# Kernel tuning notes

Hardware: AMD Instinct MI355X
Metric: run time of the kernel (lower is better)

## Reference

```python
import jax, jax.numpy as jnp
import numpy as np

DN = ('NCHW', 'OIHW', 'NCHW')

def conv3x3(x, w):
    return jax.lax.conv_general_dilated(x, w, (1, 1), ((1, 1), (1, 1)), dimension_numbers=DN)

def dsc(x, w1, w2):
    # DynamicSparseConv: per-sample per-channel softmax 3x3 depthwise kernel + residual
    B, C, H, W = x.shape
    pooled = x.mean(axis=(2, 3))                                  # [B, C] (AdaptiveAvgPool2d(1))
    h = jax.nn.gelu(pooled @ w1.T, approximate=False)             # [B, Cr] (1x1 conv == matmul)
    logits = (h @ w2.T).reshape(B, C, 9)                          # [B, C, 9]
    wk = jax.nn.softmax(logits, axis=2)
    # 3x3 patches: [B, C*9, H, W], feature dim ordered (C, kh, kw)
    patches = jax.lax.conv_general_dilated_patches(x, (3, 3), (1, 1), ((1, 1), (1, 1)))
    patches = patches.reshape(B, C, 9, H, W)
    out = jnp.einsum('bckhw,bck->bchw', patches, wk)
    return out + x

def pixel_shuffle(x, r):
    B, C, H, W = x.shape
    c = C // (r * r)
    return x.reshape(B, c, r, r, H, W).transpose(0, 1, 4, 2, 5, 3).reshape(B, c, H * r, W * r)

def setup_inputs() -> dict:
    key = jax.random.key(0)
    ks = jax.random.split(key, 12)
    B, C, H, W, OUT = 16, 128, 64, 64, 64
    CR = max(4, C // 8)            # 16
    RE = max(4, OUT // 8)          # 8
    s = 0.05
    return {
        'x1': jax.random.normal(ks[0], (B, C, H, W), jnp.float32),
        'x2': jax.random.normal(ks[1], (B, C, H, W), jnp.float32),
        'd1_w1': jax.random.normal(ks[2], (CR, C), jnp.float32) * s,
        'd1_w2': jax.random.normal(ks[3], (9 * C, CR), jnp.float32) * s,
        'd2_w1': jax.random.normal(ks[4], (CR, C), jnp.float32) * s,
        'd2_w2': jax.random.normal(ks[5], (9 * C, CR), jnp.float32) * s,
        'align_w': jax.random.normal(ks[6], (C, 2 * C), jnp.float32) * s,
        'up_w1': jax.random.normal(ks[7], (4 * C, C, 3, 3), jnp.float32) * s,
        'up_w2': jax.random.normal(ks[8], (OUT, C), jnp.float32) * s,
        're_w1': jax.random.normal(ks[9], (RE, OUT, 3, 3), jnp.float32) * s,
        're_w2': jax.random.normal(ks[10], (OUT, RE, 3, 3), jnp.float32) * s,
    }

def reference(x1, x2, d1_w1, d1_w2, d2_w1, d2_w2, align_w, up_w1, up_w2, re_w1, re_w2):
    def dynamic_block(x):  # shared weights for both inputs (same nn.Sequential)
        x = dsc(x, d1_w1, d1_w2)
        x = jax.nn.relu(x)
        return dsc(x, d2_w1, d2_w2)
    a = dynamic_block(x1)
    b = dynamic_block(x2)
    fused = jnp.einsum('bchw,oc->bohw', jnp.concatenate([a, b], axis=1), align_w)  # 1x1 conv
    u = conv3x3(fused, up_w1)            # [B, 4C, H, W]
    u = pixel_shuffle(u, 2)              # [B, C, 2H, 2W]
    up = jnp.einsum('bchw,oc->bohw', u, up_w2)  # [B, OUT, 2H, 2W]
    re = conv3x3(jax.nn.relu(conv3x3(up, re_w1)), re_w2)
    return up + re
```

## Files before the change

kernel.cpp:

```cpp
#include <hip/hip_runtime.h>
#include <math.h>

typedef unsigned short ushort;
typedef short bf16x8 __attribute__((ext_vector_type(8)));
typedef ushort us8 __attribute__((ext_vector_type(8)));
typedef float f32x16 __attribute__((ext_vector_type(16)));
typedef float f32x4 __attribute__((ext_vector_type(4)));

static const size_t OFF_POOLED = 0;
static const size_t OFF_WK     = 4096;
static const size_t OFF_WT     = 40960;
static const size_t OFF_WF     = 188416;
static const size_t OFF_AW1    = 204800;
static const size_t OFF_AW2    = 209408;
static const size_t OFF_T      = 262144;
static const size_t OFF_AB     = 8650752;
static const size_t OFF_F      = 17039360;

static __device__ __forceinline__ ushort f2bf(float f) {
    unsigned int u = __builtin_bit_cast(unsigned int, f);
    u += 0x7FFF + ((u >> 16) & 1);
    return (ushort)(u >> 16);
}
static __device__ __forceinline__ float bf2f(ushort u) {
    return __builtin_bit_cast(float, ((unsigned int)u) << 16);
}

__global__ __launch_bounds__(256) void head_kernel(const float* __restrict__ x1,
                                                   const float* __restrict__ x2,
                                                   float* __restrict__ pooled,
                                                   const float* __restrict__ up_w1,
                                                   const float* __restrict__ up_w2,
                                                   ushort* __restrict__ Awt,
                                                   const float* __restrict__ align_w,
                                                   ushort* __restrict__ Wf,
                                                   const float* __restrict__ re_w1,
                                                   ushort* __restrict__ Aw1,
                                                   const float* __restrict__ re_w2,
                                                   ushort* __restrict__ Aw2) {
    const int bid = blockIdx.x;
    const int t = threadIdx.x;
    if (bid < 4096) {
        int bc = bid;
        const float* x = (bc >> 11) ? x2 : x1;
        const float4* p = (const float4*)(x + (size_t)(bc & 2047) * 4096);
        float s = 0.f;
        for (int i = t; i < 1024; i += 256) {
            float4 v = p[i];
            s += v.x + v.y + v.z + v.w;
        }
        #pragma unroll
        for (int off = 32; off; off >>= 1) s += __shfl_down(s, off);
        __shared__ float r4[4];
        if ((t & 63) == 0) r4[t >> 6] = s;
        __syncthreads();
        if (t == 0) pooled[bc] = (r4[0] + r4[1] + r4[2] + r4[3]) * (1.f / 4096.f);
    } else if (bid < 5248) {
        int idx = (bid - 4096) * 256 + t;
        int j = idx & 7;
        int lane = (idx >> 3) & 63;
        int mt = (idx >> 9) & 3;
        int mh = (idx >> 11) & 1;
        int s = idx >> 12;
        int tap = s >> 3, c16 = s & 7;
        int arow = lane & 31;
        int o_sem = (mt & 1) * 32 + (arow & 3) + 4 * ((arow >> 3) & 3) + 16 * ((arow >> 2) & 1);
        int ph = 2 * mh + (mt >> 1);
        int cin = c16 * 16 + (lane >> 5) * 8 + j;
        float acc = 0.f;
        #pragma unroll 4
        for (int c = 0; c < 128; c++)
            acc += up_w2[o_sem * 128 + c] * up_w1[((size_t)(c * 4 + ph) * 128 + cin) * 9 + tap];
        Awt[idx] = f2bf(acc);
    } else if (bid == 5248) {
        #pragma unroll 1
        for (int i = 0; i < 16; i++) {
            int tk = t + (i << 8);
            int step = tk >> 8, mt = (tk >> 6) & 3, lane = tk & 63;
            int o = mt * 32 + (lane & 31);
            int cb = step * 16 + (lane >> 5) * 8;
            #pragma unroll
            for (int j = 0; j < 8; j++) Wf[(size_t)tk * 8 + j] = f2bf(align_w[o * 256 + cb + j]);
        }
    } else if (bid < 5285) {
        int idx = (bid - 5249) * 256 + t;
        if (idx < 9216) {
            int j = idx & 7, lane = (idx >> 3) & 63, s = idx >> 9;
            int m = lane & 15, kq = lane >> 4;
            int tap = s >> 1, ch = s & 1;
            int cin = ch * 32 + kq * 8 + j;
            float v = (m < 8) ? re_w1[((size_t)(m * 64 + cin)) * 9 + tap] : 0.f;
            Aw1[idx] = f2bf(v);
        }
    } else {
        int idx = (bid - 5285) * 256 + t;
        if (idx < 5120) {
            int j = idx & 7, lane = (idx >> 3) & 63, mt = (idx >> 9) & 1, s = idx >> 10;
            int m = mt * 32 + (lane & 31), half = lane >> 5;
            int k = s * 16 + half * 8 + j;
            int tap = k >> 3, c = k & 7;
            float v = (tap < 9) ? re_w2[((size_t)(m * 8 + c)) * 9 + tap] : 0.f;
            Aw2[idx] = f2bf(v);
        }
    }
}

__global__ __launch_bounds__(256) void dsc1_kernel(const float* __restrict__ x1,
                                                   const float* __restrict__ x2,
                                                   const float* __restrict__ pooled,
                                                   const float* __restrict__ w1,
                                                   const float* __restrict__ w2,
                                                   ushort* __restrict__ y,
                                                   float* __restrict__ pooled2) {
    int bc = blockIdx.x;
    const float* xp = ((bc >> 11) ? x2 : x1) + (size_t)(bc & 2047) * 4096;
    ushort* yp = y + (size_t)bc * 4096;
    __shared__ float tile[66 * 66];
    __shared__ float r4[4];
    __shared__ float sp[128];
    __shared__ float sh[16];
    __shared__ float lgs[9];
    int t = threadIdx.x;
    if (t < 128) sp[t] = pooled[(bc >> 7) * 128 + t];
    for (int i = t; i < 66 * 66; i += 256) tile[i] = 0.f;
    __syncthreads();
    if (t < 16) {
        float a = 0.f;
        #pragma unroll 4
        for (int c = 0; c < 128; c++) a += w1[t * 128 + c] * sp[c];
        sh[t] = 0.5f * a * (1.f + erff(a * 0.70710678118654752f));
    }
    const float4* xp4 = (const float4*)xp;
    for (int i = t; i < 1024; i += 256) {
        float4 v = xp4[i];
        int h = i >> 4, w = (i & 15) * 4;
        float* d = &tile[(h + 1) * 66 + w + 1];
        d[0] = v.x; d[1] = v.y; d[2] = v.z; d[3] = v.w;
    }
    __syncthreads();
    if (t < 9) {
        float a = 0.f;
        const float* wr = w2 + (size_t)((bc & 127) * 9 + t) * 16;
        #pragma unroll
        for (int r = 0; r < 16; r++) a += wr[r] * sh[r];
        lgs[t] = a;
    }
    __syncthreads();
    float kk[9];
    {
        float m = -INFINITY;
        #pragma unroll
        for (int k = 0; k < 9; k++) m = fmaxf(m, lgs[k]);
        float se = 0.f;
        #pragma unroll
        for (int k = 0; k < 9; k++) { kk[k] = expf(lgs[k] - m); se += kk[k]; }
        float inv = 1.f / se;
        #pragma unroll
        for (int k = 0; k < 9; k++) kk[k] *= inv;
    }
    float psum = 0.f;
    for (int i = t * 2; i < 4096; i += 512) {
        int h = i >> 6, w = i & 63;
        const float* c = &tile[h * 66 + w];
        float v0 = kk[0]*c[0] + kk[1]*c[1] + kk[2]*c[2]
                 + kk[3]*c[66] + kk[4]*c[67] + kk[5]*c[68]
                 + kk[6]*c[132] + kk[7]*c[133] + kk[8]*c[134] + c[67];
        float v1 = kk[0]*c[1] + kk[1]*c[2] + kk[2]*c[3]
                 + kk[3]*c[67] + kk[4]*c[68] + kk[5]*c[69]
                 + kk[6]*c[133] + kk[7]*c[134] + kk[8]*c[135] + c[68];
        v0 = fmaxf(v0, 0.f); v1 = fmaxf(v1, 0.f);
        psum += v0 + v1;
        ushort2 pk = {f2bf(v0), f2bf(v1)};
        *(ushort2*)&yp[i] = pk;
    }
    #pragma unroll
    for (int off = 32; off; off >>= 1) psum += __shfl_down(psum, off);
    if ((t & 63) == 0) r4[t >> 6] = psum;
    __syncthreads();
    if (t == 0) pooled2[bc] = (r4[0] + r4[1] + r4[2] + r4[3]) * (1.f / 4096.f);
}

__global__ __launch_bounds__(256) void dsc2_kernel(const ushort* __restrict__ x,
                                                   const float* __restrict__ pooled,
                                                   const float* __restrict__ w1,
                                                   const float* __restrict__ w2,
                                                   ushort* __restrict__ y) {
    int bc = blockIdx.x;
    const ushort* xp = x + (size_t)bc * 4096;
    ushort* yp = y + (size_t)bc * 4096;
    __shared__ float tile[66 * 66];
    __shared__ float sp[128];
    __shared__ float sh[16];
    __shared__ float lgs[9];
    int t = threadIdx.x;
    if (t < 128) sp[t] = pooled[(bc >> 7) * 128 + t];
    for (int i = t; i < 66 * 66; i += 256) tile[i] = 0.f;
    __syncthreads();
    if (t < 16) {
        float a = 0.f;
        #pragma unroll 4
        for (int c = 0; c < 128; c++) a += w1[t * 128 + c] * sp[c];
        sh[t] = 0.5f * a * (1.f + erff(a * 0.70710678118654752f));
    }
    for (int i = t; i < 512; i += 256) {
        int4 raw = *(const int4*)&xp[i * 8];
        const ushort* u = (const ushort*)&raw;
        int h = i >> 3, w = (i & 7) * 8;
        float* d = &tile[(h + 1) * 66 + w + 1];
        #pragma unroll
        for (int j = 0; j < 8; j++) d[j] = bf2f(u[j]);
    }
    __syncthreads();
    if (t < 9) {
        float a = 0.f;
        const float* wr = w2 + (size_t)((bc & 127) * 9 + t) * 16;
        #pragma unroll
        for (int r = 0; r < 16; r++) a += wr[r] * sh[r];
        lgs[t] = a;
    }
    __syncthreads();
    float kk[9];
    {
        float m = -INFINITY;
        #pragma unroll
        for (int k = 0; k < 9; k++) m = fmaxf(m, lgs[k]);
        float se = 0.f;
        #pragma unroll
        for (int k = 0; k < 9; k++) { kk[k] = expf(lgs[k] - m); se += kk[k]; }
        float inv = 1.f / se;
        #pragma unroll
        for (int k = 0; k < 9; k++) kk[k] *= inv;
    }
    for (int i = t * 2; i < 4096; i += 512) {
        int h = i >> 6, w = i & 63;
        const float* c = &tile[h * 66 + w];
        float v0 = kk[0]*c[0] + kk[1]*c[1] + kk[2]*c[2]
                 + kk[3]*c[66] + kk[4]*c[67] + kk[5]*c[68]
                 + kk[6]*c[132] + kk[7]*c[133] + kk[8]*c[134] + c[67];
        float v1 = kk[0]*c[1] + kk[1]*c[2] + kk[2]*c[3]
                 + kk[3]*c[67] + kk[4]*c[68] + kk[5]*c[69]
                 + kk[6]*c[133] + kk[7]*c[134] + kk[8]*c[135] + c[68];
        ushort2 pk = {f2bf(v0), f2bf(v1)};
        *(ushort2*)&yp[i] = pk;
    }
}

__global__ __launch_bounds__(256, 2) void align_mfma_kernel(const ushort* __restrict__ A,
                                                            const ushort* __restrict__ Bv,
                                                            const ushort* __restrict__ Wf,
                                                            ushort* __restrict__ F) {
    __shared__ ushort Xs[2 * 128 * 8];
    const int b = blockIdx.y;
    const int px0 = blockIdx.x << 7;
    const int tid = threadIdx.x;
    const int wave = tid >> 6, lane = tid & 63;
    const int l31 = lane & 31, half = lane >> 5;

    f32x16 acc[4];
    #pragma unroll
    for (int mt = 0; mt < 4; mt++)
        #pragma unroll
        for (int r = 0; r < 16; r++) acc[mt][r] = 0.f;

    const int cg0 = tid >> 7, pxs0 = tid & 127;
    const int bfofs = (wave * 32 + l31) * 8 + half * 1024;

    for (int step = 0; step < 16; step++) {
        const ushort* src =
            (step < 8 ? A : Bv) + (((size_t)(b * 128 + (step & 7) * 16)) << 12) + px0;
        if (step) __syncthreads();
        #pragma unroll
        for (int q = 0; q < 2; q++) {
            int cg = cg0 + q * 2, px = pxs0;
            ushort v0 = src[((size_t)(cg * 4 + 0) << 12) + px];
            ushort v1 = src[((size_t)(cg * 4 + 1) << 12) + px];
            ushort v2 = src[((size_t)(cg * 4 + 2) << 12) + px];
            ushort v3 = src[((size_t)(cg * 4 + 3) << 12) + px];
            ushort4 pk = {v0, v1, v2, v3};
            *(ushort4*)&Xs[(cg >> 1) * 1024 + px * 8 + (cg & 1) * 4] = pk;
        }
        __syncthreads();
        bf16x8 bfrag = *(const bf16x8*)&Xs[bfofs];
        const bf16x8* wf = (const bf16x8*)(Wf + ((size_t)step * 4 * 64 + lane) * 8);
        #pragma unroll
        for (int mt = 0; mt < 4; mt++)
            acc[mt] = __builtin_amdgcn_mfma_f32_32x32x16_bf16(wf[mt * 64], bfrag, acc[mt], 0, 0, 0);
    }
    ushort* fp = F + ((size_t)(b * 4096 + px0 + wave * 32 + l31)) * 128;
    #pragma unroll
    for (int mt = 0; mt < 4; mt++) {
        #pragma unroll
        for (int g = 0; g < 4; g++) {
            ushort4 pk = {f2bf(acc[mt][g * 4 + 0]), f2bf(acc[mt][g * 4 + 1]),
                          f2bf(acc[mt][g * 4 + 2]), f2bf(acc[mt][g * 4 + 3])};
            *(ushort4*)(fp + mt * 32 + half * 4 + 8 * g) = pk;
        }
    }
}

__global__ __launch_bounds__(512, 4) void up_mfma_kernel(const ushort* __restrict__ F,
                                                         const ushort* __restrict__ Awt,
                                                         ushort* __restrict__ U) {
    __shared__ ushort Xs[180 * 128];
    const int b = blockIdx.y;
    const int tr = blockIdx.x >> 3, tc = blockIdx.x & 7;
    const int tid = threadIdx.x;
    const int wave = tid >> 6, lane = tid & 63;
    const int l31 = lane & 31, half = lane >> 5;
    const int mh = wave >> 2, bmt = (wave >> 1) & 1, nh = wave & 1;

    for (int idx = tid; idx < 2880; idx += 512) {
        int px = idx >> 4, q = idx & 15;
        int r = px / 10, c = px - r * 10;
        int gh = tr * 16 - 1 + r, gw = tc * 8 - 1 + c;
        int4 v = {0, 0, 0, 0};
        if ((unsigned)gh < 64u && (unsigned)gw < 64u)
            v = *(const int4*)(F + ((size_t)(b * 4096 + gh * 64 + gw)) * 128 + q * 8);
        *(int4*)&Xs[px * 128 + ((q ^ (px & 7)) << 3)] = v;
    }
    __syncthreads();

    f32x16 acc[2][2];
    #pragma unroll
    for (int mt = 0; mt < 2; mt++)
        #pragma unroll
        for (int nt = 0; nt < 2; nt++)
            #pragma unroll
            for (int r = 0; r < 16; r++) acc[mt][nt][r] = 0.f;

    int xpos[2];
    #pragma unroll
    for (int nt = 0; nt < 2; nt++) {
        int pxl = nh * 64 + nt * 32 + l31;
        xpos[nt] = (pxl >> 3) * 10 + (pxl & 7);
    }

    const ushort* abase = Awt + (size_t)(mh * 4 + bmt * 2) * 512 + lane * 8;

    #define LDA(ss, mtl) (*(const bf16x8*)(abase + (size_t)(ss) * 4096 + (mtl) * 512))
    #define LDB(ss, nt) ({                                                   \
        int tap_ = (ss) >> 3, c16_ = (ss) & 7;                               \
        int ky_ = (tap_ * 11) >> 5;                      \
        int kx_ = tap_ - ky_ * 3;                                            \
        int p_ = xpos[nt] + ky_ * 10 + kx_;                                  \
        int qq_ = c16_ * 2 + half;                                           \
        *(const bf16x8*)&Xs[p_ * 128 + ((qq_ ^ (p_ & 7)) << 3)];             \
    })

    bf16x8 A0[2], A1[2], B0[2], B1[2];
    A0[0] = LDA(0, 0); A0[1] = LDA(0, 1);
    A1[0] = LDA(1, 0); A1[1] = LDA(1, 1);
    B0[0] = LDB(0, 0); B0[1] = LDB(0, 1);
    B1[0] = LDB(1, 0); B1[1] = LDB(1, 1);

    #define SUBSTEP(ASET, BSET, sn)                                                  \
    {                                                                                \
        _Pragma("unroll")                                                            \
        for (int mt = 0; mt < 2; mt++) {                                             \
            acc[mt][0] = __builtin_amdgcn_mfma_f32_32x32x16_bf16(ASET[mt], BSET[0], acc[mt][0], 0, 0, 0); \
            acc[mt][1] = __builtin_amdgcn_mfma_f32_32x32x16_bf16(ASET[mt], BSET[1], acc[mt][1], 0, 0, 0); \
        }                                                                            \
        ASET[0] = LDA(sn, 0); ASET[1] = LDA(sn, 1);                                  \
        BSET[0] = LDB(sn, 0); BSET[1] = LDB(sn, 1);                                  \
    }

    #pragma unroll 2
    for (int s = 0; s < 70; s += 2) {
        SUBSTEP(A0, B0, s + 2)
        int s3 = (s + 3 < 72) ? s + 3 : 0;
        SUBSTEP(A1, B1, s3)
    }
    #pragma unroll
    for (int mt = 0; mt < 2; mt++) {
        acc[mt][0] = __builtin_amdgcn_mfma_f32_32x32x16_bf16(A0[mt], B0[0], acc[mt][0], 0, 0, 0);
        acc[mt][1] = __builtin_amdgcn_mfma_f32_32x32x16_bf16(A0[mt], B0[1], acc[mt][1], 0, 0, 0);
    }
    #pragma unroll
    for (int mt = 0; mt < 2; mt++) {
        acc[mt][0] = __builtin_amdgcn_mfma_f32_32x32x16_bf16(A1[mt], B1[0], acc[mt][0], 0, 0, 0);
        acc[mt][1] = __builtin_amdgcn_mfma_f32_32x32x16_bf16(A1[mt], B1[1], acc[mt][1], 0, 0, 0);
    }
    #undef SUBSTEP
    #undef LDA
    #undef LDB

    #pragma unroll
    for (int nt = 0; nt < 2; nt++) {
        int pxl = nh * 64 + nt * 32 + l31;
        int Y = 2 * (tr * 16 + (pxl >> 3)) + mh;
        int X = 2 * (tc * 8 + (pxl & 7)) + bmt;
        #pragma unroll
        for (int mt = 0; mt < 2; mt++) {
            ushort* up = U + ((size_t)((b * 128 + Y) * 128 + X)) * 64
                       + mt * 32 + half * 16;
            us8 p0, p1;
            #pragma unroll
            for (int i = 0; i < 8; i++) {
                p0[i] = f2bf(acc[mt][nt][i]);
                p1[i] = f2bf(acc[mt][nt][8 + i]);
            }
            *(us8*)up = p0;
            *(us8*)(up + 8) = p1;
        }
    }
}

__global__ __launch_bounds__(256, 2) void re1_kernel(const ushort* __restrict__ U,
                                                     const ushort* __restrict__ Aw1,
                                                     ushort* __restrict__ R1) {
    __shared__ ushort Xs[324 * 72];
    __shared__ ushort As[18 * 64 * 8];
    const int b = blockIdx.y;
    const int ty = blockIdx.x >> 3, tx = blockIdx.x & 7;
    const int tid = threadIdx.x;
    const int wave = tid >> 6, lane = tid & 63;
    const int m16 = lane & 15, kq = lane >> 4;

    for (int idx = tid; idx < 1152; idx += 256)
        *(int4*)&As[idx * 8] = *(const int4*)(Aw1 + (size_t)idx * 8);
    for (int idx = tid; idx < 2592; idx += 256) {
        int px = idx >> 3, q = idx & 7;
        int r = px / 18, c = px - r * 18;
        int gY = ty * 16 - 1 + r, gX = tx * 16 - 1 + c;
        int4 v = {0, 0, 0, 0};
        if ((unsigned)gY < 128u && (unsigned)gX < 128u)
            v = *(const int4*)(U + ((size_t)((b * 128 + gY) * 128 + gX)) * 64 + q * 8);
        *(int4*)&Xs[px * 72 + q * 8] = v;
    }
    __syncthreads();

    f32x4 acc[4];
    #pragma unroll
    for (int nt = 0; nt < 4; nt++)
        #pragma unroll
        for (int r = 0; r < 4; r++) acc[nt][r] = 0.f;

    #pragma unroll 1
    for (int s = 0; s < 18; s++) {
        bf16x8 a = *(const bf16x8*)&As[(s * 64 + lane) * 8];
        int tap = s >> 1, ch = s & 1;
        int ky = tap / 3, kx = tap - ky * 3;
        int xo = (ky * 18 + kx) * 72 + ch * 32 + kq * 8;
        #pragma unroll
        for (int nt = 0; nt < 4; nt++) {
            int row = wave * 4 + nt;
            bf16x8 bv = *(const bf16x8*)&Xs[(row * 18 + m16) * 72 + xo];
            acc[nt] = __builtin_amdgcn_mfma_f32_16x16x32_bf16(a, bv, acc[nt], 0, 0, 0);
        }
    }
    if (kq < 2) {
        #pragma unroll
        for (int nt = 0; nt < 4; nt++) {
            int gY = ty * 16 + wave * 4 + nt, gX = tx * 16 + m16;
            ushort4 pk = {f2bf(fmaxf(acc[nt][0], 0.f)), f2bf(fmaxf(acc[nt][1], 0.f)),
                          f2bf(fmaxf(acc[nt][2], 0.f)), f2bf(fmaxf(acc[nt][3], 0.f))};
            *(ushort4*)(R1 + ((size_t)((b * 128 + gY) * 128 + gX)) * 8 + kq * 4) = pk;
        }
    }
}

__global__ __launch_bounds__(256, 2) void re2_kernel(const ushort* __restrict__ R1,
                                                     const ushort* __restrict__ U,
                                                     const ushort* __restrict__ Aw2,
                                                     float* __restrict__ out) {
    __shared__ ushort Xs[324 * 8];
    __shared__ ushort As[5 * 2 * 64 * 8];
    __shared__ ushort Us[256 * 68];
    const int b = blockIdx.y;
    const int ty = blockIdx.x >> 3, tx = blockIdx.x & 7;
    const int tid = threadIdx.x;
    const int wave = tid >> 6, lane = tid & 63;
    const int l31 = lane & 31, half = lane >> 5;

    for (int idx = tid; idx < 640; idx += 256)
        *(int4*)&As[idx * 8] = *(const int4*)(Aw2 + (size_t)idx * 8);
    for (int idx = tid; idx < 324; idx += 256) {
        int r = idx / 18, c = idx - r * 18;
        int gY = ty * 16 - 1 + r, gX = tx * 16 - 1 + c;
        int4 v = {0, 0, 0, 0};
        if ((unsigned)gY < 128u && (unsigned)gX < 128u)
            v = *(const int4*)(R1 + ((size_t)((b * 128 + gY) * 128 + gX)) * 8);
        *(int4*)&Xs[idx * 8] = v;
    }
    for (int idx = tid; idx < 2048; idx += 256) {
        int px = idx >> 3, q = idx & 7;
        int gY = ty * 16 + (px >> 4), gX = tx * 16 + (px & 15);
        const ushort* s = U + ((size_t)((b * 128 + gY) * 128 + gX)) * 64 + q * 8;
        ushort4 v0 = *(const ushort4*)s;
        ushort4 v1 = *(const ushort4*)(s + 4);
        *(ushort4*)&Us[px * 68 + q * 8] = v0;
        *(ushort4*)&Us[px * 68 + q * 8 + 4] = v1;
    }
    __syncthreads();

    f32x16 acc[2][2];
    #pragma unroll
    for (int mt = 0; mt < 2; mt++)
        #pragma unroll
        for (int nt = 0; nt < 2; nt++)
            #pragma unroll
            for (int r = 0; r < 16; r++) acc[mt][nt][r] = 0.f;

    #pragma unroll
    for (int s = 0; s < 5; s++) {
        bf16x8 a0 = *(const bf16x8*)&As[((s * 2 + 0) * 64 + lane) * 8];
        bf16x8 a1 = *(const bf16x8*)&As[((s * 2 + 1) * 64 + lane) * 8];
        int t = 2 * s + half;
        if (t > 8) t = 8;
        int ky = t / 3, kx = t - ky * 3;
        #pragma unroll
        for (int nt = 0; nt < 2; nt++) {
            int pxl = wave * 64 + nt * 32 + l31;
            int row = pxl >> 4, col = pxl & 15;
            bf16x8 bv = *(const bf16x8*)&Xs[((row + ky) * 18 + col + kx) * 8];
            acc[0][nt] = __builtin_amdgcn_mfma_f32_32x32x16_bf16(a0, bv, acc[0][nt], 0, 0, 0);
            acc[1][nt] = __builtin_amdgcn_mfma_f32_32x32x16_bf16(a1, bv, acc[1][nt], 0, 0, 0);
        }
    }
    #pragma unroll
    for (int mt = 0; mt < 2; mt++) {
        #pragma unroll
        for (int nt = 0; nt < 2; nt++) {
            int pxl = wave * 64 + nt * 32 + l31;
            int gY = ty * 16 + (pxl >> 4), gX = tx * 16 + (pxl & 15);
            #pragma unroll
            for (int r = 0; r < 16; r++) {
                int o = mt * 32 + (r & 3) + 8 * (r >> 2) + 4 * half;
                float v = acc[mt][nt][r] + bf2f(Us[pxl * 68 + o]);
                out[((size_t)(b * 64 + o) * 128 + gY) * 128 + gX] = v;
            }
        }
    }
}

extern "C" void kernel_launch(void* const* d_in, const int* in_sizes, int n_in,
                              void* d_out, int out_size, void* d_ws, size_t ws_size,
                              hipStream_t stream) {
    const float* x1      = (const float*)d_in[0];
    const float* x2      = (const float*)d_in[1];
    const float* d1_w1   = (const float*)d_in[2];
    const float* d1_w2   = (const float*)d_in[3];
    const float* d2_w1   = (const float*)d_in[4];
    const float* d2_w2   = (const float*)d_in[5];
    const float* align_w = (const float*)d_in[6];
    const float* up_w1   = (const float*)d_in[7];
    const float* up_w2   = (const float*)d_in[8];
    const float* re_w1   = (const float*)d_in[9];
    const float* re_w2   = (const float*)d_in[10];
    float* out = (float*)d_out;
    float* ws  = (float*)d_ws;

    float*  pooled  = ws + OFF_POOLED;
    float*  pooled2 = ws + OFF_WK;
    ushort* Awt    = (ushort*)(ws + OFF_WT);
    ushort* Wf     = (ushort*)(ws + OFF_WF);
    ushort* Aw1    = (ushort*)(ws + OFF_AW1);
    ushort* Aw2    = (ushort*)(ws + OFF_AW2);
    ushort* bufT   = (ushort*)(ws + OFF_T);
    ushort* R1     = (ushort*)(ws + OFF_T);
    ushort* bufAB  = (ushort*)(ws + OFF_AB);
    ushort* bufU   = (ushort*)(ws + OFF_AB);
    ushort* F      = (ushort*)(ws + OFF_F);

    head_kernel<<<5305, 256, 0, stream>>>(x1, x2, pooled, up_w1, up_w2, Awt,
                                          align_w, Wf, re_w1, Aw1, re_w2, Aw2);
    dsc1_kernel<<<4096, 256, 0, stream>>>(x1, x2, pooled, d1_w1, d1_w2, bufT, pooled2);
    dsc2_kernel<<<4096, 256, 0, stream>>>(bufT, pooled2, d2_w1, d2_w2, bufAB);

    align_mfma_kernel<<<dim3(32, 16), 256, 0, stream>>>(bufAB, bufAB + 8388608, Wf, F);
    up_mfma_kernel<<<dim3(32, 16), 512, 0, stream>>>(F, Awt, bufU);
    re1_kernel<<<dim3(64, 16), 256, 0, stream>>>(bufU, Aw1, R1);
    re2_kernel<<<dim3(64, 16), 256, 0, stream>>>(R1, bufU, Aw2, out);
}
```

Baseline: 328.3 us.

## Stage weight-fold operands in LDS and compute eight outputs per thread

The head kernel's up_w2×up_w1 weight-folding section is rewritten so each block stages the relevant up_w2 rows and a tap-specific slice of up_w1 into shared memory, then each thread accumulates eight outputs from LDS instead of doing strided global loads per output. This cuts the block count for that section from 1152 to 144 and removes the redundant, uncoalesced global reads. In exchange every head block now declares about 48KB of shared memory, which may reduce occupancy for the pooling blocks that share the kernel. Each block also reads up_w1 with a filter that discards most loaded values.

```diff
diff --git a/kernel.cpp b/kernel.cpp
--- a/kernel.cpp
+++ b/kernel.cpp
@@ -38,6 +38,7 @@
                                                    ushort* __restrict__ Aw1,
                                                    const float* __restrict__ re_w2,
                                                    ushort* __restrict__ Aw2) {
+    __shared__ float sm[12352];
     const int bid = blockIdx.x;
     const int t = threadIdx.x;
     if (bid < 4096) {
@@ -51,28 +52,52 @@
         }
         #pragma unroll
         for (int off = 32; off; off >>= 1) s += __shfl_down(s, off);
-        __shared__ float r4[4];
-        if ((t & 63) == 0) r4[t >> 6] = s;
+        if ((t & 63) == 0) sm[t >> 6] = s;
         __syncthreads();
-        if (t == 0) pooled[bc] = (r4[0] + r4[1] + r4[2] + r4[3]) * (1.f / 4096.f);
-    } else if (bid < 5248) {
-        int idx = (bid - 4096) * 256 + t;
-        int j = idx & 7;
-        int lane = (idx >> 3) & 63;
-        int mt = (idx >> 9) & 3;
-        int mh = (idx >> 11) & 1;
-        int s = idx >> 12;
+        if (t == 0) pooled[bc] = (sm[0] + sm[1] + sm[2] + sm[3]) * (1.f / 4096.f);
+    } else if (bid < 4240) {
+        int w = bid - 4096;
+        int mh = (w >= 72) ? 1 : 0;
+        int s = w - mh * 72;
         int tap = s >> 3, c16 = s & 7;
-        int arow = lane & 31;
-        int o_sem = (mt & 1) * 32 + (arow & 3) + 4 * ((arow >> 3) & 3) + 16 * ((arow >> 2) & 1);
-        int ph = 2 * mh + (mt >> 1);
-        int cin = c16 * 16 + (lane >> 5) * 8 + j;
-        float acc = 0.f;
+        float* W2s = sm;
+        float* W1s = sm + 8256;
+        for (int i = t; i < 8192; i += 256)
+            W2s[(i >> 7) * 129 + (i & 127)] = up_w2[i];
+        for (int i = t; i < 36864; i += 256) {
+            int r_idx = i / 144;
+            int k = i - r_idx * 144;
+            int r = ((r_idx >> 1) << 2) + 2 * mh + (r_idx & 1);
+            float v = up_w1[(size_t)r * 1152 + c16 * 144 + k];
+            int cin_l = k / 9;
+            int tp = k - cin_l * 9;
+            if (tp == tap) W1s[r_idx * 16 + cin_l] = v;
+        }
+        __syncthreads();
+        float accv[8];
+        int wb[8], xb[8];
+        #pragma unroll
+        for (int oi = 0; oi < 8; oi++) {
+            accv[oi] = 0.f;
+            int L8 = oi * 256 + t;
+            int j = L8 & 7;
+            int lane = (L8 >> 3) & 63;
+            int mt = (L8 >> 9) & 3;
+            int arow = lane & 31;
+            int o_sem = (mt & 1) * 32 + (arow & 3) + 4 * ((arow >> 3) & 3) + 16 * ((arow >> 2) & 1);
+            wb[oi] = o_sem * 129;
+            xb[oi] = (mt >> 1) * 16 + ((lane >> 5) << 3) + j;
+        }
         #pragma unroll 4
-        for (int c = 0; c < 128; c++)
-            acc += up_w2[o_sem * 128 + c] * up_w1[((size_t)(c * 4 + ph) * 128 + cin) * 9 + tap];
-        Awt[idx] = f2bf(acc);
-    } else if (bid == 5248) {
+        for (int c = 0; c < 128; c++) {
+            #pragma unroll
+            for (int oi = 0; oi < 8; oi++)
+                accv[oi] += W2s[wb[oi] + c] * W1s[c * 32 + xb[oi]];
+        }
+        #pragma unroll
+        for (int oi = 0; oi < 8; oi++)
+            Awt[(size_t)s * 4096 + mh * 2048 + oi * 256 + t] = f2bf(accv[oi]);
+    } else if (bid == 4240) {
         #pragma unroll 1
         for (int i = 0; i < 16; i++) {
             int tk = t + (i << 8);
@@ -82,8 +107,8 @@
             #pragma unroll
             for (int j = 0; j < 8; j++) Wf[(size_t)tk * 8 + j] = f2bf(align_w[o * 256 + cb + j]);
         }
-    } else if (bid < 5285) {
-        int idx = (bid - 5249) * 256 + t;
+    } else if (bid < 4277) {
+        int idx = (bid - 4241) * 256 + t;
         if (idx < 9216) {
             int j = idx & 7, lane = (idx >> 3) & 63, s = idx >> 9;
             int m = lane & 15, kq = lane >> 4;
@@ -93,7 +118,7 @@
             Aw1[idx] = f2bf(v);
         }
     } else {
-        int idx = (bid - 5285) * 256 + t;
+        int idx = (bid - 4277) * 256 + t;
         if (idx < 5120) {
             int j = idx & 7, lane = (idx >> 3) & 63, mt = (idx >> 9) & 1, s = idx >> 10;
             int m = mt * 32 + (lane & 31), half = lane >> 5;
@@ -562,7 +587,7 @@
     ushort* bufU   = (ushort*)(ws + OFF_AB);
     ushort* F      = (ushort*)(ws + OFF_F);
 
-    head_kernel<<<5305, 256, 0, stream>>>(x1, x2, pooled, up_w1, up_w2, Awt,
+    head_kernel<<<4297, 256, 0, stream>>>(x1, x2, pooled, up_w1, up_w2, Awt,
                                           align_w, Wf, re_w1, Aw1, re_w2, Aw2);
     dsc1_kernel<<<4096, 256, 0, stream>>>(x1, x2, pooled, d1_w1, d1_w2, bufT, pooled2);
     dsc2_kernel<<<4096, 256, 0, stream>>>(bufT, pooled2, d2_w1, d2_w2, bufAB);
```

Result: slower. 380.2 us (+15.8%).
